# Performance work log

Hardware: AMD Instinct MI355X
Metric: run time of the kernel (lower is better)

Reference implementation:

```python
import jax, jax.numpy as jnp
import numpy as np

TEMP = 2.0      # softmax temperature
POOL_K = 0.5    # node keep ratio
BN_EPS = 1e-5


def setup_inputs() -> dict:
    key = jax.random.key(0)
    ks = jax.random.split(key, 8)
    bs, n, d = 8, 512, 64
    return {
        "x": jax.random.normal(ks[0], (bs, n, d), jnp.float32),
        "att_w": jax.random.normal(ks[1], (d, d), jnp.float32) / np.sqrt(d),
        "att_b": jnp.zeros((d,), jnp.float32),
        "att_weight": jax.random.normal(ks[2], (d, 1), jnp.float32) / np.sqrt(d),
        "pwa_w": jax.random.normal(ks[3], (d, d), jnp.float32) / np.sqrt(d),
        "pwa_b": jnp.zeros((d,), jnp.float32),
        "pwo_w": jax.random.normal(ks[4], (d, d), jnp.float32) / np.sqrt(d),
        "pwo_b": jnp.zeros((d,), jnp.float32),
        "gamma": jnp.ones((d,), jnp.float32),
        "beta": jnp.zeros((d,), jnp.float32),
        "rmean": jnp.zeros((d,), jnp.float32),
        "rvar": jnp.ones((d,), jnp.float32),
        "pool_w": jax.random.normal(ks[5], (d, 1), jnp.float32) / np.sqrt(d),
        "pool_b": jnp.zeros((1,), jnp.float32),
    }


def reference(x, att_w, att_b, att_weight, pwa_w, pwa_b, pwo_w, pwo_b,
              gamma, beta, rmean, rvar, pool_w, pool_b):
    # --- GraphAttentionLayer (eval mode: dropout = identity) ---
    # pairwise node products: (b, n, n, d)
    pair = x[:, :, None, :] * x[:, None, :, :]
    # tanh(Linear(pair)) then contract with att_weight -> logits (b, n, n)
    t = jnp.tanh(jnp.einsum('bijd,de->bije', pair, att_w) + att_b)
    logits = jnp.einsum('bijd,d->bij', t, att_weight[:, 0]) / TEMP
    # softmax over dim=-2 of (b,n,n,1) == axis 2 here
    attn = jax.nn.softmax(logits, axis=2)           # (b, n, n)
    agg = jnp.einsum('bij,bjd->bid', attn, x)       # attended features
    h = (agg @ pwa_w + pwa_b) + (x @ pwo_w + pwo_b)
    # BatchNorm1d, eval mode over flattened (b*n, d)
    h = (h - rmean) * jax.lax.rsqrt(rvar + BN_EPS) * gamma + beta
    h = jax.nn.selu(h)

    # --- GraphPool (eval mode: dropout = identity) ---
    scores = jax.nn.sigmoid(h @ pool_w + pool_b)    # (b, n, 1)
    n_keep = max(int(h.shape[1] * POOL_K), 1)
    _, idx = jax.lax.top_k(scores[..., 0], n_keep)  # (b, n_keep), desc sorted
    hs = h * scores
    out = jnp.take_along_axis(hs, idx[..., None], axis=1)  # (b, n_keep, d)
    return out
```

## Files before the change

### kernel.cpp

```cpp
#include <hip/hip_runtime.h>

#define NB 8
#define NN 512
#define ND 64
#define NKEEP 256
#define PJ 132
#define WSCALE 2.8853900817779268f
#define K2 0.72134752f

#define SELU_SCALE 1.0507009873554805f
#define SELU_ALPHA 1.6732632423543773f

typedef __attribute__((ext_vector_type(8))) short short8;
typedef __attribute__((ext_vector_type(4))) float f32x4;

__device__ __forceinline__ unsigned short f2bf_rne(float f) {
    unsigned u = __float_as_uint(f);
    return (unsigned short)((u + 0x7fffu + ((u >> 16) & 1u)) >> 16);
}
__device__ __forceinline__ float bf2f(unsigned short h) {
    return __uint_as_float(((unsigned)h) << 16);
}

__device__ __forceinline__ void gl2lds16(const unsigned short* g, unsigned short* l) {
    __builtin_amdgcn_global_load_lds(
        (const __attribute__((address_space(1))) unsigned int*)g,
        (__attribute__((address_space(3))) unsigned int*)l,
        16, 0, 0);
}
__device__ __forceinline__ void gl2lds16f(const float* g, float* l) {
    __builtin_amdgcn_global_load_lds(
        (const __attribute__((address_space(1))) unsigned int*)g,
        (__attribute__((address_space(3))) unsigned int*)l,
        16, 0, 0);
}

__device__ __forceinline__ unsigned pack2(float a, float b) {
    return (unsigned)f2bf_rne(a) | ((unsigned)f2bf_rne(b) << 16);
}
__device__ __forceinline__ unsigned pack2lo(float a, unsigned short ha,
                                            float b, unsigned short hb) {
    unsigned la = __float_as_uint(a - bf2f(ha)) >> 16;
    unsigned lb = __float_as_uint(b - bf2f(hb)) & 0xffff0000u;
    return la | lb;
}

__device__ __forceinline__ void cvt_store_pair(float4 va, float4 vb,
                                               unsigned short* Xh,
                                               unsigned short* Xl, int idx) {
    unsigned short h0 = f2bf_rne(va.x), h1 = f2bf_rne(va.y),
                   h2 = f2bf_rne(va.z), h3 = f2bf_rne(va.w),
                   h4 = f2bf_rne(vb.x), h5 = f2bf_rne(vb.y),
                   h6 = f2bf_rne(vb.z), h7 = f2bf_rne(vb.w);
    uint4 hw, lw;
    hw.x = (unsigned)h0 | ((unsigned)h1 << 16);
    hw.y = (unsigned)h2 | ((unsigned)h3 << 16);
    hw.z = (unsigned)h4 | ((unsigned)h5 << 16);
    hw.w = (unsigned)h6 | ((unsigned)h7 << 16);
    lw.x = pack2lo(va.x, h0, va.y, h1);
    lw.y = pack2lo(va.z, h2, va.w, h3);
    lw.z = pack2lo(vb.x, h4, vb.y, h5);
    lw.w = pack2lo(vb.z, h6, vb.w, h7);
    *(uint4*)(&Xh[idx]) = hw;
    *(uint4*)(&Xl[idx]) = lw;
}

__global__ __launch_bounds__(512, 4)
void sast_logit_kernel(const float* __restrict__ x,
                       const float* __restrict__ att_w,
                       const float* __restrict__ att_b,
                       const float* __restrict__ att_wt,
                       unsigned short* __restrict__ p_buf)
{
    __shared__ alignas(16) unsigned short Xh[8192];
    __shared__ alignas(16) unsigned short Xl[8192];
    __shared__ float probs[4 * PJ];
    __shared__ float lpP[4 * PJ];
    __shared__ float xg[4 * ND];

    const int tid  = threadIdx.x;
    const int w    = tid >> 6;
    const int iw   = w & 3;
    const int eh   = w >> 2;
    const int lane = tid & 63;
    const int g    = lane >> 4;
    const int rr   = lane & 15;
    const int rnd  = blockIdx.x >> 8;
    const int m0   = blockIdx.x & 31;
    const int m    = (rnd & 1) ? (31 - m0) : m0;
    const int b    = (blockIdx.x >> 5) & 7;
    const int i0   = 128 * rnd + 4 * m;
    const int c0   = rnd;

    const float* xf = x + b * NN * ND;
    unsigned short* pb = p_buf + b * NN * NN;

    const int rj = tid >> 2;
    const int q0 = (tid & 3) * 4;
    const int sw = (rj & 7) << 3;
    const int cidx0 = rj * 64 + (((q0 + 0) * 4) ^ sw);
    const int cidx1 = rj * 64 + (((q0 + 2) * 4) ^ sw);

    float sab = 0.f;
    #pragma unroll
    for (int e4 = 0; e4 < ND; e4 += 4) {
        float4 awv = *(const float4*)(att_wt + e4);
        sab += fabsf(awv.x) + fabsf(awv.y) + fabsf(awv.z) + fabsf(awv.w);
    }
    const float nLam2 = -K2 * sab;

    const int swz = (rr & 7) << 3;
    const int fb0 = rr * 64 + ((g * 8) ^ swz);
    const int fb1 = rr * 64 + ((g * 8 + 32) ^ swz);

    if (tid < 256) xg[tid] = x[(b * NN + i0 + (tid >> 6)) * ND + (tid & 63)];

    {
        const float* src = xf + (c0 * 128 + rj) * ND + q0 * 4;
        float4 v0 = *(const float4*)(src);
        float4 v1 = *(const float4*)(src + 4);
        float4 v2 = *(const float4*)(src + 8);
        float4 v3 = *(const float4*)(src + 12);
        cvt_store_pair(v0, v1, Xh, Xl, cidx0);
        cvt_store_pair(v2, v3, Xh, Xl, cidx1);
    }
    __syncthreads();

    short8 Wh[2][2], Wl[2][2];
    #pragma unroll
    for (int mt2 = 0; mt2 < 2; ++mt2) {
        const int mt = eh * 2 + mt2;
        #pragma unroll
        for (int ks = 0; ks < 2; ++ks) {
            #pragma unroll
            for (int t = 0; t < 8; ++t) {
                int d = ks * 32 + g * 8 + t;
                int e = mt * 16 + rr;
                float wv = att_w[d * ND + e] * xg[iw * ND + d] * WSCALE;
                unsigned short hh = f2bf_rne(wv);
                unsigned short ll = (unsigned short)(__float_as_uint(wv - bf2f(hh)) >> 16);
                Wh[mt2][ks][t] = (short)hh;
                Wl[mt2][ks][t] = (short)ll;
            }
        }
    }
    f32x4 attb4[2], mw4[2];
    float basep = 0.f;
    #pragma unroll
    for (int mt2 = 0; mt2 < 2; ++mt2) {
        const int mt = eh * 2 + mt2;
        #pragma unroll
        for (int r = 0; r < 4; ++r) {
            int e = mt * 16 + g * 4 + r;
            float aw = att_wt[e];
            attb4[mt2][r] = att_b[e] * WSCALE;
            mw4[mt2][r]   = -2.0f * aw;
            basep += aw;
        }
    }

    for (int c = c0; c < 4; ++c) {
        const int jb = c << 7;
        const int jt0 = (i0 > jb) ? ((i0 - jb) >> 4) : 0;

        float lp_own[8];
        #pragma unroll
        for (int jt = jt0; jt < 8; ++jt) {
            short8 bh0 = *(const short8*)(Xh + fb0 + jt * 1024);
            short8 bh1 = *(const short8*)(Xh + fb1 + jt * 1024);
            short8 bl0 = *(const short8*)(Xl + fb0 + jt * 1024);
            short8 bl1 = *(const short8*)(Xl + fb1 + jt * 1024);
            float lp = basep;
            #pragma unroll
            for (int mt2 = 0; mt2 < 2; ++mt2) {
                f32x4 acc = attb4[mt2];
                acc = __builtin_amdgcn_mfma_f32_16x16x32_bf16(Wh[mt2][0], bh0, acc, 0, 0, 0);
                acc = __builtin_amdgcn_mfma_f32_16x16x32_bf16(Wh[mt2][1], bh1, acc, 0, 0, 0);
                acc = __builtin_amdgcn_mfma_f32_16x16x32_bf16(Wh[mt2][0], bl0, acc, 0, 0, 0);
                acc = __builtin_amdgcn_mfma_f32_16x16x32_bf16(Wh[mt2][1], bl1, acc, 0, 0, 0);
                acc = __builtin_amdgcn_mfma_f32_16x16x32_bf16(Wl[mt2][0], bh0, acc, 0, 0, 0);
                acc = __builtin_amdgcn_mfma_f32_16x16x32_bf16(Wl[mt2][1], bh1, acc, 0, 0, 0);
                f32x4 mw = mw4[mt2];
                float u0 = exp2f(fminf(acc[0], 60.f));
                float u1 = exp2f(fminf(acc[1], 60.f));
                float u2 = exp2f(fminf(acc[2], 60.f));
                float u3 = exp2f(fminf(acc[3], 60.f));
                float n01 = fmaf(mw[0], u1, fmaf(mw[1], u0, mw[0] + mw[1]));
                float d01 = fmaf(u0, u1, 1.0f + (u0 + u1));
                float n23 = fmaf(mw[2], u3, fmaf(mw[3], u2, mw[2] + mw[3]));
                float d23 = fmaf(u2, u3, 1.0f + (u2 + u3));
                lp = fmaf(n01, __builtin_amdgcn_rcpf(d01), lp);
                lp = fmaf(n23, __builtin_amdgcn_rcpf(d23), lp);
            }
            lp += __shfl_xor(lp, 16);
            lp += __shfl_xor(lp, 32);
            if (eh == 0) lp_own[jt] = lp;
            else if (lane < 16) lpP[iw * PJ + jt * 16 + rr] = lp;
        }
        __syncthreads();

        float4 v0, v1, v2, v3;
        if (c < 3) {
            const float* src = xf + ((c + 1) * 128 + rj) * ND + q0 * 4;
            v0 = *(const float4*)(src);
            v1 = *(const float4*)(src + 4);
            v2 = *(const float4*)(src + 8);
            v3 = *(const float4*)(src + 12);
        }

        if (eh == 0 && lane < 16) {
            #pragma unroll
            for (int jt = jt0; jt < 8; ++jt) {
                float t = lp_own[jt] + lpP[iw * PJ + jt * 16 + rr];
                probs[iw * PJ + jt * 16 + rr] = exp2f(fmaf(t, K2, nLam2));
            }
        }

        if (c < 3) {
            cvt_store_pair(v0, v1, Xh, Xl, cidx0);
            cvt_store_pair(v2, v3, Xh, Xl, cidx1);
        }
        __syncthreads();

        {
            const int iw2 = tid >> 7, jl = tid & 127, j = jb + jl;
            if (j >= i0) {
                float p = fminf(probs[iw2 * PJ + jl], 1.0f);
                pb[(i0 + iw2) * NN + j] =
                    (unsigned short)__float2uint_rn(p * 65535.f);
            }
        }
    }
}

__global__ __launch_bounds__(1024, 2)
void sast_agg_kernel(const float* __restrict__ x,
                     const unsigned short* __restrict__ p_buf,
                     const float* __restrict__ pwa_w,
                     const float* __restrict__ pwa_b,
                     const float* __restrict__ pwo_w,
                     const float* __restrict__ pwo_b,
                     const float* __restrict__ gma,
                     const float* __restrict__ bta,
                     const float* __restrict__ rmean,
                     const float* __restrict__ rvar,
                     const float* __restrict__ pool_w,
                     const float* __restrict__ pool_b,
                     float* __restrict__ ws_h,
                     float* __restrict__ ws_score)
{
    __shared__ alignas(16) float Xc[8192];
    __shared__ alignas(16) unsigned short prow[16 * NN];
    __shared__ alignas(16) unsigned short pcolT[NN * 16];
    __shared__ float xrow[16 * ND];
    __shared__ float aggsh[16 * ND];

    const int tid  = threadIdx.x;
    const int w    = tid >> 6;
    const int lane = tid & 63;
    const int b    = blockIdx.x >> 5;
    const int i0   = (blockIdx.x & 31) * 16;
    const int i    = i0 + w;
    const float* xb = x + b * NN * ND;
    const unsigned short* pbb = p_buf + b * NN * NN;

    gl2lds16(pbb + i * NN + (lane << 3), &prow[w << 9]);
    gl2lds16f(xb + w * 512 +       (lane << 2), &Xc[w * 512]);
    gl2lds16f(xb + w * 512 + 256 + (lane << 2), &Xc[w * 512 + 256]);
    for (int t = tid; t < i0 + 12; t += 1024) {
        *(uint4*)(&pcolT[t * 16])     = *(const uint4*)(pbb + t * NN + i0);
        *(uint4*)(&pcolT[t * 16 + 8]) = *(const uint4*)(pbb + t * NN + i0 + 8);
    }
    xrow[tid] = xb[i0 * ND + tid];
    __syncthreads();

    const int B = i0 + (w & ~3);
    for (int j = lane; j < B; j += 64)
        prow[(w << 9) + j] = pcolT[j * 16 + w];

    uint4 q = *(const uint4*)(&prow[(w << 9) + (lane << 3)]);
    unsigned us = (q.x & 0xffffu) + (q.x >> 16) + (q.y & 0xffffu) + (q.y >> 16)
                + (q.z & 0xffffu) + (q.z >> 16) + (q.w & 0xffffu) + (q.w >> 16);
    #pragma unroll
    for (int m = 32; m; m >>= 1) us += (unsigned)__shfl_xor((int)us, m);
    const float Sinv = __fdividef(1.0f, (float)us);

    float acc0 = 0.f, acc1 = 0.f;
    for (int c = 0; c < 4; ++c) {
        if (c) {
            __syncthreads();
            gl2lds16f(xb + c * 8192 + w * 512 +       (lane << 2), &Xc[w * 512]);
            gl2lds16f(xb + c * 8192 + w * 512 + 256 + (lane << 2), &Xc[w * 512 + 256]);
            __syncthreads();
        }
        const int jb = c << 7;
        #pragma unroll 4
        for (int jl = 0; jl < 128; jl += 2) {
            unsigned pu = *(const unsigned*)(&prow[(w << 9) + jb + jl]);
            acc0 = fmaf((float)(pu & 0xffffu), Xc[jl * 64 + lane], acc0);
            acc1 = fmaf((float)(pu >> 16),     Xc[(jl + 1) * 64 + lane], acc1);
        }
    }
    aggsh[w * ND + lane] = (acc0 + acc1) * Sinv;

    float hv = pwa_b[lane] + pwo_b[lane];
    #pragma unroll 4
    for (int d = 0; d < ND; ++d)
        hv = fmaf(aggsh[w * ND + d], pwa_w[d * ND + lane],
             fmaf(xrow[w * ND + d], pwo_w[d * ND + lane], hv));
    hv = (hv - rmean[lane]) * rsqrtf(rvar[lane] + 1e-5f) * gma[lane] + bta[lane];
    hv = hv > 0.f ? SELU_SCALE * hv
                  : SELU_SCALE * SELU_ALPHA * (__expf(hv) - 1.0f);
    ws_h[(b * NN + i) * ND + lane] = hv;
    float sc = hv * pool_w[lane];
    #pragma unroll
    for (int m = 32; m; m >>= 1) sc += __shfl_xor(sc, m);
    if (lane == 0)
        ws_score[b * NN + i] = __fdividef(1.0f, 1.0f + __expf(-(sc + pool_b[0])));
}

__global__ void sast_topk_kernel(const float* __restrict__ ws_h,
                                 const float* __restrict__ ws_score,
                                 float* __restrict__ out)
{
    __shared__ float s[NN];
    __shared__ int sel[NKEEP];
    const int b = blockIdx.x, tid = threadIdx.x;
    s[tid] = ws_score[b * NN + tid];
    __syncthreads();
    const float v = s[tid];
    int rank = 0;
    for (int j = 0; j < NN; ++j) {
        float sj = s[j];
        rank += ((sj > v) || (sj == v && j < tid)) ? 1 : 0;
    }
    if (rank < NKEEP) sel[rank] = tid;
    __syncthreads();
    #pragma unroll
    for (int it = 0; it < NKEEP * ND / 512; ++it) {
        int f = it * 512 + tid;
        int k = f >> 6, e = f & 63;
        int j = sel[k];
        out[(b * NKEEP + k) * ND + e] = ws_h[(b * NN + j) * ND + e] * s[j];
    }
}

extern "C" void kernel_launch(void* const* d_in, const int* in_sizes, int n_in,
                              void* d_out, int out_size, void* d_ws, size_t ws_size,
                              hipStream_t stream)
{
    const float* x      = (const float*)d_in[0];
    const float* att_w  = (const float*)d_in[1];
    const float* att_b  = (const float*)d_in[2];
    const float* att_wt = (const float*)d_in[3];
    const float* pwa_w  = (const float*)d_in[4];
    const float* pwa_b  = (const float*)d_in[5];
    const float* pwo_w  = (const float*)d_in[6];
    const float* pwo_b  = (const float*)d_in[7];
    const float* gma    = (const float*)d_in[8];
    const float* bta    = (const float*)d_in[9];
    const float* rmean  = (const float*)d_in[10];
    const float* rvar   = (const float*)d_in[11];
    const float* pool_w = (const float*)d_in[12];
    const float* pool_b = (const float*)d_in[13];
    float* out   = (float*)d_out;
    float* ws_h  = (float*)d_ws;
    float* ws_sc = ws_h + NB * NN * ND;
    unsigned short* p_buf = (unsigned short*)(ws_sc + NB * NN);

    sast_logit_kernel<<<NB * 128, 512, 0, stream>>>(
        x, att_w, att_b, att_wt, p_buf);
    sast_agg_kernel<<<NB * 32, 1024, 0, stream>>>(
        x, p_buf, pwa_w, pwa_b, pwo_w, pwo_b,
        gma, bta, rmean, rvar, pool_w, pool_b, ws_h, ws_sc);
    sast_topk_kernel<<<NB, 512, 0, stream>>>(ws_h, ws_sc, out);
}
```

Measured before the change: 89.41 us.

## Parallelize top-k rank computation across 8 blocks per batch with split scans

The top-k kernel now launches 8 blocks per batch instead of one. Each node's rank is computed by 8 threads that each scan 64 scores and combine their counts with shuffles. Each selected node's row is then scattered directly to its output slot with float4 loads and stores, so the shared selection array and second barrier are gone. This shortens the serial 512-iteration rank loop in a tiny 8-block launch, at the cost of every block reloading that batch's full score array.

Result: faster. 77.35 us (-13.5%).

```diff
diff --git a/kernel.cpp b/kernel.cpp
--- a/kernel.cpp
+++ b/kernel.cpp
@@ -35,9 +35,6 @@
         16, 0, 0);
 }
 
-__device__ __forceinline__ unsigned pack2(float a, float b) {
-    return (unsigned)f2bf_rne(a) | ((unsigned)f2bf_rne(b) << 16);
-}
 __device__ __forceinline__ unsigned pack2lo(float a, unsigned short ha,
                                             float b, unsigned short hb) {
     unsigned la = __float_as_uint(a - bf2f(ha)) >> 16;
@@ -319,29 +316,39 @@
         ws_score[b * NN + i] = __fdividef(1.0f, 1.0f + __expf(-(sc + pool_b[0])));
 }
 
-__global__ void sast_topk_kernel(const float* __restrict__ ws_h,
-                                 const float* __restrict__ ws_score,
-                                 float* __restrict__ out)
+__global__ __launch_bounds__(512)
+void sast_topk_kernel(const float* __restrict__ ws_h,
+                      const float* __restrict__ ws_score,
+                      float* __restrict__ out)
 {
     __shared__ float s[NN];
-    __shared__ int sel[NKEEP];
-    const int b = blockIdx.x, tid = threadIdx.x;
+    const int tid = threadIdx.x;
+    const int b   = blockIdx.x >> 3;
+    const int g   = blockIdx.x & 7;
     s[tid] = ws_score[b * NN + tid];
     __syncthreads();
-    const float v = s[tid];
+    const int c    = tid >> 3;
+    const int part = tid & 7;
+    const int i    = g * 64 + c;
+    const float v  = s[i];
     int rank = 0;
-    for (int j = 0; j < NN; ++j) {
+    #pragma unroll 8
+    for (int j = part * 64; j < part * 64 + 64; ++j) {
         float sj = s[j];
-        rank += ((sj > v) || (sj == v && j < tid)) ? 1 : 0;
-    }
-    if (rank < NKEEP) sel[rank] = tid;
-    __syncthreads();
-    #pragma unroll
-    for (int it = 0; it < NKEEP * ND / 512; ++it) {
-        int f = it * 512 + tid;
-        int k = f >> 6, e = f & 63;
-        int j = sel[k];
-        out[(b * NKEEP + k) * ND + e] = ws_h[(b * NN + j) * ND + e] * s[j];
+        rank += ((sj > v) || (sj == v && j < i)) ? 1 : 0;
+    }
+    rank += __shfl_xor(rank, 1);
+    rank += __shfl_xor(rank, 2);
+    rank += __shfl_xor(rank, 4);
+    if (rank < NKEEP) {
+        const float* src = ws_h + (b * NN + i) * ND + part * 8;
+        float* dst = out + (b * NKEEP + rank) * ND + part * 8;
+        float4 a0 = *(const float4*)(src);
+        float4 a1 = *(const float4*)(src + 4);
+        a0.x *= v; a0.y *= v; a0.z *= v; a0.w *= v;
+        a1.x *= v; a1.y *= v; a1.z *= v; a1.w *= v;
+        *(float4*)(dst)     = a0;
+        *(float4*)(dst + 4) = a1;
     }
 }
 
@@ -373,5 +380,5 @@
     sast_agg_kernel<<<NB * 32, 1024, 0, stream>>>(
         x, p_buf, pwa_w, pwa_b, pwo_w, pwo_b,
         gma, bta, rmean, rvar, pool_w, pool_b, ws_h, ws_sc);
-    sast_topk_kernel<<<NB, 512, 0, stream>>>(ws_h, ws_sc, out);
-}
+    sast_topk_kernel<<<NB * 8, 512, 0, stream>>>(ws_h, ws_sc, out);
+}
```
